# Performance work log

Hardware: AMD Instinct MI355X
Metric: run time of the kernel (lower is better)

The kernel has to match this reference:

```python
import jax, jax.numpy as jnp
import numpy as np

B, T, C, L = 1024, 256, 100, 64  # batch, time steps, classes (blank=C-1), label length
NEG = -1e30   # safe -inf for log-space DP
EPS = 1e-7    # Keras K.epsilon() added before log


def setup_inputs() -> dict:
    key = jax.random.key(0)
    k1, k2 = jax.random.split(key)
    logits = jax.random.normal(k1, (B, T, C), dtype=jnp.float32)
    y_pred = jax.nn.softmax(logits, axis=-1)  # ctc_batch_cost expects probabilities
    y_true = jax.random.randint(k2, (B, L), 0, C - 1)  # labels in [0, C-2]; blank=C-1
    return {"y_true": y_true, "y_pred": y_pred}


def ctc_loss(y_true, y_pred):
    """Faithful K.ctc_batch_cost with full input/label lengths, blank = C-1."""
    Bb, Tt, Cc = y_pred.shape
    Ll = y_true.shape[1]
    S = 2 * Ll + 1  # extended label lattice: blank-interleaved
    blank = Cc - 1

    # extended labels: [blank, l0, blank, l1, ..., blank]
    ext = jnp.full((Bb, S), blank, dtype=y_true.dtype).at[:, 1::2].set(y_true)
    # skip-transition allowed when ext[s] is non-blank and differs from ext[s-2]
    ext_m2 = jnp.concatenate([jnp.full((Bb, 2), -1, ext.dtype), ext[:, :-2]], axis=1)
    allow = (ext != blank) & (ext != ext_m2)  # [B,S]

    logp = jnp.log(y_pred + EPS)  # [B,T,C]
    # gather log-probs on the lattice once: [B,T,S]
    lp_ext = jnp.take_along_axis(
        logp, jnp.broadcast_to(ext[:, None, :], (Bb, Tt, S)), axis=2)
    lp_seq = jnp.moveaxis(lp_ext, 1, 0)  # [T,B,S] for scan

    # alpha init: only states 0 (blank) and 1 (first label) reachable at t=0
    alpha0 = jnp.where(jnp.arange(S)[None, :] < 2, lp_seq[0], NEG)

    def shift(a, k):
        return jnp.concatenate(
            [jnp.full((Bb, k), NEG, a.dtype), a[:, :-k]], axis=1)

    def step(alpha, lp_t):
        new = jnp.logaddexp(
            jnp.logaddexp(alpha, shift(alpha, 1)),
            jnp.where(allow, shift(alpha, 2), NEG)) + lp_t
        return new, None

    alphaT, _ = jax.lax.scan(step, alpha0, lp_seq[1:])
    # total prob = alpha[T-1, S-1] + alpha[T-1, S-2]
    loss = -jnp.logaddexp(alphaT[:, -1], alphaT[:, -2])
    return loss[:, None]  # ctc_batch_cost returns shape [B,1]


def reference(y_true, y_pred):
    return ctc_loss(y_true, y_pred)
```

## Files before the change

kernel.cpp:

```cpp
#include <hip/hip_runtime.h>

#define B_ 1024
#define T_ 256
#define C_ 100
#define L_ 64
#define EPS_ 1e-7f
#define LN2 0.69314718055994530942f

#define LOG2F(x) __builtin_amdgcn_logf(x)

__device__ __forceinline__ float dpp_shr1(float x) {
    return __int_as_float(__builtin_amdgcn_update_dpp(
        0, __float_as_int(x), 0x138, 0xf, 0xf, false));
}

#define STEP(pb_, pl_) do {                                               \
    const float up1 = dpp_shr1(a1);                                       \
    const float s   = allow ? up1 : 0.0f;                                 \
    const float n0  = (a0 + up1) * (pb_);                                 \
    const float n1  = ((a1 + a0) + s) * (pl_);                            \
    const float n2  = (a2 + a1) * (pb_);                                  \
    a0 = n0; a1 = n1; a2 = n2;                                            \
} while (0)

#define PLAN() do {                                                       \
    float m_ = fmaxf(fmaxf(a0, a1), a2);                                  \
    _Pragma("unroll")                                                     \
    for (int d_ = 1; d_ < 64; d_ <<= 1) m_ = fmaxf(m_, __shfl_xor(m_, d_)); \
    const int e_ = (__float_as_int(m_) >> 23) & 255;                      \
    rs_K = 127 - e_;                                                      \
    rs_scale = __int_as_float((254 - e_) << 23);           \
} while (0)

#define APPLY() do { a0 *= rs_scale; a1 *= rs_scale; a2 *= rs_scale;      \
                     Sacc += rs_K; } while (0)

__global__ __launch_bounds__(64) void ctc_kernel(
    const int* __restrict__ y_true,
    const float* __restrict__ y_pred,
    float* __restrict__ out)
{
    const int b    = blockIdx.x;
    const int lane = threadIdx.x;

    const float* __restrict__ base = y_pred + (size_t)b * T_ * C_;
    const int label   = y_true[b * L_ + lane];
    const int labprev = __shfl_up(label, 1);
    const bool allow  = (lane == 0) || (label != labprev);

    const float* __restrict__ pL = base + label;
    const float* __restrict__ pB = base + (C_ - 1);

    float pl[2][16], pb[2][16];

    #pragma unroll
    for (int k = 0; k < 16; ++k) { pl[0][k] = pL[k * C_];        pb[0][k] = pB[k * C_]; }
    #pragma unroll
    for (int k = 0; k < 16; ++k) { pl[1][k] = pL[(16 + k) * C_]; pb[1][k] = pB[(16 + k) * C_]; }

    float a0 = 0.0f, a1 = 0.0f, a2 = 0.0f;
    float rs_scale = 1.0f;
    int   rs_K = 0, Sacc = 0;

    #pragma unroll
    for (int c = 0; c < 16; ++c) {
        if (c >= 1 && c + 1 < 16) {
            #pragma unroll
            for (int k = 0; k < 16; ++k) {
                pl[(c + 1) & 1][k] = pL[((c + 1) * 16 + k) * C_];
                pb[(c + 1) & 1][k] = pB[((c + 1) * 16 + k) * C_];
            }
        }
        #pragma unroll
        for (int k = 0; k < 16; ++k) {
            if (c == 0 && k == 0) {
                a0 = (lane == 0) ? (pb[0][0] + EPS_) : 0.0f;
                a1 = (lane == 0) ? (pl[0][0] + EPS_) : 0.0f;
                a2 = 0.0f;
                PLAN();
            } else {
                if (k == 0 || k == 8) {
                    APPLY();
                    PLAN();
                }
                STEP(pb[c & 1][k] + EPS_, pl[c & 1][k] + EPS_);
            }
        }
    }

    if (lane == 63) {
        out[b] = -LN2 * (LOG2F(a1 + a2) - (float)Sacc);
    }
}

extern "C" void kernel_launch(void* const* d_in, const int* in_sizes, int n_in,
                              void* d_out, int out_size, void* d_ws, size_t ws_size,
                              hipStream_t stream) {
    const int*   y_true = (const int*)d_in[0];
    const float* y_pred = (const float*)d_in[1];
    float*       out    = (float*)d_out;

    ctc_kernel<<<dim3(B_), dim3(64), 0, stream>>>(y_true, y_pred, out);
}
```

Before: 28.32 us.

## Stream lattice probabilities through LDS with async global_load_lds pipeline

Replaces register double-buffered 16-step loads with a 4-slot LDS ring filled by global_load_lds in chunks of 8 time steps, three chunks in flight, paced by explicit s_waitcnt vmcnt counts. The goal is to cut register pressure and keep more loads outstanding, hiding global latency behind the serial DP recurrence. The blank probabilities for a chunk are loaded once (one per lane) and read back as LDS broadcasts. The cost is extra LDS reads per step and a dependence on hand-counted vmcnt values; there is no barrier, which is acceptable only because the block is a single wavefront.

Measured after the change: 24.01 us. 1.18x faster.

```diff
diff --git a/kernel.cpp b/kernel.cpp
--- a/kernel.cpp
+++ b/kernel.cpp
@@ -7,7 +7,18 @@
 #define EPS_ 1e-7f
 #define LN2 0.69314718055994530942f
 
+#define CH 8
+#define NCH (T_ / CH)
+#define DEPTH 3
+
 #define LOG2F(x) __builtin_amdgcn_logf(x)
+
+typedef const __attribute__((address_space(1))) void GV;
+typedef __attribute__((address_space(3))) void LV;
+
+__device__ __forceinline__ void gload_lds4(const void* g, void* l) {
+    __builtin_amdgcn_global_load_lds((GV*)g, (LV*)l, 4, 0, 0);
+}
 
 __device__ __forceinline__ float dpp_shr1(float x) {
     return __int_as_float(__builtin_amdgcn_update_dpp(
@@ -35,11 +46,22 @@
 #define APPLY() do { a0 *= rs_scale; a1 *= rs_scale; a2 *= rs_scale;      \
                      Sacc += rs_K; } while (0)
 
+#define ISSUE(c_) do {                                                    \
+    const int bufi_ = (c_) & 3;                                           \
+    _Pragma("unroll")                                                     \
+    for (int j_ = 0; j_ < CH; ++j_)                                       \
+        gload_lds4(pL + ((c_) * CH + j_) * C_, &plbuf[bufi_][j_][0]);     \
+    gload_lds4(pBl + (c_) * CH * C_, &pbbuf[bufi_][0]);                   \
+} while (0)
+
 __global__ __launch_bounds__(64) void ctc_kernel(
     const int* __restrict__ y_true,
     const float* __restrict__ y_pred,
     float* __restrict__ out)
 {
+    __shared__ float plbuf[4][CH][64];
+    __shared__ float pbbuf[4][64];
+
     const int b    = blockIdx.x;
     const int lane = threadIdx.x;
 
@@ -48,44 +70,39 @@
     const int labprev = __shfl_up(label, 1);
     const bool allow  = (lane == 0) || (label != labprev);
 
-    const float* __restrict__ pL = base + label;
-    const float* __restrict__ pB = base + (C_ - 1);
+    const float* __restrict__ pL  = base + label;
+    const float* __restrict__ pBl = base + (C_ - 1) + (lane & (CH - 1)) * C_;
 
-    float pl[2][16], pb[2][16];
-
-    #pragma unroll
-    for (int k = 0; k < 16; ++k) { pl[0][k] = pL[k * C_];        pb[0][k] = pB[k * C_]; }
-    #pragma unroll
-    for (int k = 0; k < 16; ++k) { pl[1][k] = pL[(16 + k) * C_]; pb[1][k] = pB[(16 + k) * C_]; }
+    ISSUE(0); ISSUE(1); ISSUE(2);
 
     float a0 = 0.0f, a1 = 0.0f, a2 = 0.0f;
     float rs_scale = 1.0f;
     int   rs_K = 0, Sacc = 0;
 
     #pragma unroll
-    for (int c = 0; c < 16; ++c) {
-        if (c >= 1 && c + 1 < 16) {
+    for (int c = 0; c < NCH; ++c) {
+        if (c <= NCH - 3)      { asm volatile("s_waitcnt vmcnt(18)" ::: "memory"); }
+        else if (c == NCH - 2) { asm volatile("s_waitcnt vmcnt(9)"  ::: "memory"); }
+        else                   { asm volatile("s_waitcnt vmcnt(0)"  ::: "memory"); }
+
+        const int bufi = c & 3;
+        if (c == 0) {
+            a0 = (lane == 0) ? (pbbuf[0][0] + EPS_) : 0.0f;
+            a1 = (lane == 0) ? (plbuf[0][0][lane] + EPS_) : 0.0f;
+            a2 = 0.0f;
+            PLAN();
             #pragma unroll
-            for (int k = 0; k < 16; ++k) {
-                pl[(c + 1) & 1][k] = pL[((c + 1) * 16 + k) * C_];
-                pb[(c + 1) & 1][k] = pB[((c + 1) * 16 + k) * C_];
-            }
+            for (int j = 1; j < CH; ++j)
+                STEP(pbbuf[bufi][j] + EPS_, plbuf[bufi][j][lane] + EPS_);
+        } else {
+            APPLY();
+            PLAN();
+            #pragma unroll
+            for (int j = 0; j < CH; ++j)
+                STEP(pbbuf[bufi][j] + EPS_, plbuf[bufi][j][lane] + EPS_);
         }
-        #pragma unroll
-        for (int k = 0; k < 16; ++k) {
-            if (c == 0 && k == 0) {
-                a0 = (lane == 0) ? (pb[0][0] + EPS_) : 0.0f;
-                a1 = (lane == 0) ? (pl[0][0] + EPS_) : 0.0f;
-                a2 = 0.0f;
-                PLAN();
-            } else {
-                if (k == 0 || k == 8) {
-                    APPLY();
-                    PLAN();
-                }
-                STEP(pb[c & 1][k] + EPS_, pl[c & 1][k] + EPS_);
-            }
-        }
+
+        if (c + DEPTH < NCH) ISSUE(c + DEPTH);
     }
 
     if (lane == 63) {
```
